# Optimization experiments

Measured on AMD Instinct MI355X. Metric: run time of the kernel, lower is better.

The kernel has to match this reference:

```python
import jax, jax.numpy as jnp
import numpy as np

B, S, H = 2, 1024, 1024        # batch, seq, hidden_size
E, I = 16, 512                 # n_routed_experts, moe_intermediate_size
TOP_K = 2                      # num_experts_per_tok
N_SHARED = 2                   # n_shared_experts -> shared intermediate = I * N_SHARED
SCALE = 1.0                    # routed_scaling_factor
IS = I * N_SHARED


def setup_inputs() -> dict:
    key = jax.random.key(0)
    ks = jax.random.split(key, 8)
    sd = 0.02
    return {
        "hidden_states": jax.random.normal(ks[0], (B, S, H), jnp.float32),
        "gate_w": jax.random.normal(ks[1], (E, H), jnp.float32) * sd,   # router weight [E, H]
        "w_gate": jax.random.normal(ks[2], (E, H, I), jnp.float32) * sd,
        "w_up":   jax.random.normal(ks[3], (E, H, I), jnp.float32) * sd,
        "w_down": jax.random.normal(ks[4], (E, I, H), jnp.float32) * sd,
        "ws_gate": jax.random.normal(ks[5], (H, IS), jnp.float32) * sd,
        "ws_up":   jax.random.normal(ks[6], (H, IS), jnp.float32) * sd,
        "ws_down": jax.random.normal(ks[7], (IS, H), jnp.float32) * sd,
    }


def reference(hidden_states, gate_w, w_gate, w_up, w_down, ws_gate, ws_up, ws_down):
    b, s, h = hidden_states.shape
    x = hidden_states.reshape(-1, h)                      # [T, H]
    T = x.shape[0]

    # ---- gate (greedy top-k over softmax of router logits, fp32) ----
    logits = jnp.einsum('th,eh->te', x.astype(jnp.float32), gate_w.astype(jnp.float32))
    scores = jax.nn.softmax(logits, axis=-1)              # [T, E]
    topk_w, topk_idx = jax.lax.top_k(scores, TOP_K)       # [T, K]
    topk_w = topk_w * SCALE

    # combine weights as dense [T, E] (equivalent to argsort dispatch + scatter combine)
    combine = jnp.zeros((T, E), jnp.float32).at[
        jnp.arange(T)[:, None], topk_idx].add(topk_w)     # [T, E]

    # ---- routed experts: SwiGLU MLP per expert, weighted combine ----
    g = jnp.einsum('th,ehi->tei', x, w_gate)              # [T, E, I]
    u = jnp.einsum('th,ehi->tei', x, w_up)                # [T, E, I]
    act = jax.nn.silu(g) * u                              # [T, E, I]
    # fuse down-proj with combine weights to avoid a [T, E, H] intermediate
    routed = jnp.einsum('tei,eih,te->th', act, w_down, combine)  # [T, H]

    # ---- shared experts on the residual ----
    sg = jax.nn.silu(x @ ws_gate) * (x @ ws_up)           # [T, IS]
    shared = sg @ ws_down                                 # [T, H]

    return (routed + shared).reshape(b, s, h)
```

## Files before the change

### kernel.cpp

```cpp
#include <hip/hip_runtime.h>
#include <hip/hip_bf16.h>

#define T_TOK 2048
#define H_DIM 1024
#define NEXP  16
#define I_DIM 512
#define CAP   384
#define RSCALE 1.0f

typedef unsigned short u16;
typedef unsigned int   u32;
typedef __attribute__((ext_vector_type(4))) float  f32x4;
typedef __attribute__((ext_vector_type(8))) __bf16 bf16x8;
typedef __attribute__((ext_vector_type(8))) u16    u16x8;
typedef __attribute__((ext_vector_type(4))) u16    u16x4;

__device__ __forceinline__ u16 f2bf(float f) {
  u32 u = __builtin_bit_cast(u32, f);
  u32 r = u + 0x7fffu + ((u >> 16) & 1u);
  return (u16)(r >> 16);
}
__device__ __forceinline__ float bf2f(u16 h) {
  return __builtin_bit_cast(float, (u32)h << 16);
}
__device__ __forceinline__ void gload16(const void* g, void* l) {
  __builtin_amdgcn_global_load_lds((const __attribute__((address_space(1))) u32*)g,
                                   (__attribute__((address_space(3))) u32*)l, 16, 0, 0);
}

__device__ __forceinline__ void transpose_tile(const float* __restrict__ src, int srcN,
                                               int k0, int n0,
                                               u16* __restrict__ dst, int dstride, int drow0)
{
  __shared__ float t[64][65];
  int tid = threadIdx.x;
  int kl = tid >> 4, c4 = (tid & 15) * 4;
  #pragma unroll
  for (int p = 0; p < 4; ++p) {
    f32x4 v = *(const f32x4*)(src + (size_t)(k0 + p*16 + kl) * srcN + n0 + c4);
    #pragma unroll
    for (int j = 0; j < 4; ++j) t[p*16 + kl][c4 + j] = v[j];
  }
  __syncthreads();
  int nl = tid >> 3, kc = (tid & 7) * 8;
  #pragma unroll
  for (int p = 0; p < 2; ++p) {
    int n = p*32 + nl;
    u16x8 o;
    #pragma unroll
    for (int j = 0; j < 8; ++j) o[j] = f2bf(t[kc + j][n]);
    *(u16x8*)(dst + (size_t)(drow0 + n) * dstride + k0 + kc) = o;
  }
}

__global__ __launch_bounds__(256) void convert_kernel(
    const float* __restrict__ x,
    const float* __restrict__ w_gate, const float* __restrict__ w_up,
    const float* __restrict__ w_down,
    const float* __restrict__ wsg, const float* __restrict__ wsu,
    const float* __restrict__ wsd,
    u16* __restrict__ xb, u16* __restrict__ wgu_t, u16* __restrict__ wd_t,
    u16* __restrict__ wsgu_t, u16* __restrict__ wsd_t)
{
  int tile = blockIdx.x, tid = threadIdx.x;
  if (tile < 512) {
    #pragma unroll
    for (int p = 0; p < 4; ++p) {
      int fi = tile*1024 + p*256 + tid;
      f32x4 v = ((const f32x4*)x)[fi];
      u16x4 o;
      #pragma unroll
      for (int j = 0; j < 4; ++j) o[j] = f2bf(v[j]);
      ((u16x4*)xb)[fi] = o;
    }
  } else if (tile < 4608) {
    int t2 = tile - 512; int e = t2 >> 8; int r = t2 & 255;
    int mat = r >> 7; int q = r & 127; int kt = q >> 3, nt = q & 7;
    const float* src = (mat ? w_up : w_gate) + (size_t)e * H_DIM * I_DIM;
    transpose_tile(src, I_DIM, kt*64, nt*64,
                   wgu_t + (size_t)e * 1024 * 1024, 1024, mat*512 + nt*64);
  } else if (tile < 6656) {
    int t2 = tile - 4608; int e = t2 >> 7; int q = t2 & 127;
    int kt = q >> 4, nt = q & 15;
    transpose_tile(w_down + (size_t)e * I_DIM * H_DIM, H_DIM, kt*64, nt*64,
                   wd_t + (size_t)e * 1024 * 512, 512, nt*64);
  } else if (tile < 7168) {
    int t2 = tile - 6656; int mat = t2 >> 8; int q = t2 & 255;
    int kt = q >> 4, nt = q & 15;
    transpose_tile(mat ? wsu : wsg, 1024, kt*64, nt*64,
                   wsgu_t, 1024, mat*1024 + nt*64);
  } else {
    int t2 = tile - 7168; int kt = t2 >> 4, nt = t2 & 15;
    transpose_tile(wsd, H_DIM, kt*64, nt*64, wsd_t, 1024, nt*64);
  }
}

__global__ __launch_bounds__(256) void router_kernel(
    const float* __restrict__ x, const float* __restrict__ gw,
    int* __restrict__ perm_tok, int* __restrict__ slot_of,
    float* __restrict__ tok_w, int* __restrict__ counts)
{
  __shared__ f32x4 gws[4096];
  int tid = threadIdx.x;
  const f32x4* gw4 = (const f32x4*)gw;
  #pragma unroll
  for (int i = 0; i < 16; ++i) gws[i*256 + tid] = gw4[i*256 + tid];
  __syncthreads();

  int wv = tid >> 6, l = tid & 63;
  int t0 = blockIdx.x * 16 + wv * 4;

  f32x4 xv[4][4];
  #pragma unroll
  for (int tk = 0; tk < 4; ++tk) {
    const f32x4* xr = (const f32x4*)(x + (size_t)(t0 + tk) * H_DIM);
    #pragma unroll
    for (int j = 0; j < 4; ++j) xv[tk][j] = xr[j*64 + l];
  }

  float p[4][NEXP];
  #pragma unroll
  for (int tk = 0; tk < 4; ++tk)
    #pragma unroll
    for (int e = 0; e < NEXP; ++e) p[tk][e] = 0.f;

  #pragma unroll
  for (int j = 0; j < 4; ++j)
    #pragma unroll
    for (int e = 0; e < NEXP; ++e) {
      f32x4 g = gws[e*256 + j*64 + l];
      #pragma unroll
      for (int tk = 0; tk < 4; ++tk)
        p[tk][e] += xv[tk][j][0]*g[0] + xv[tk][j][1]*g[1]
                  + xv[tk][j][2]*g[2] + xv[tk][j][3]*g[3];
    }

  #pragma unroll
  for (int tk = 0; tk < 4; ++tk)
    #pragma unroll
    for (int e = 0; e < NEXP; ++e)
      #pragma unroll
      for (int off = 32; off; off >>= 1)
        p[tk][e] += __shfl_xor(p[tk][e], off);

  if (l < 4) {
    int tk = l;
    int t = t0 + tk;
    float m = p[tk][0];
    #pragma unroll
    for (int e = 1; e < NEXP; ++e) m = fmaxf(m, p[tk][e]);
    float q[NEXP]; float s = 0.f;
    #pragma unroll
    for (int e = 0; e < NEXP; ++e) { q[e] = expf(p[tk][e] - m); s += q[e]; }
    float inv = 1.f / s;
    int e1 = 0; float b1 = -1.f;
    #pragma unroll
    for (int e = 0; e < NEXP; ++e) if (q[e] > b1) { b1 = q[e]; e1 = e; }
    int e2 = -1; float b2 = -1.f;
    #pragma unroll
    for (int e = 0; e < NEXP; ++e) if (e != e1 && q[e] > b2) { b2 = q[e]; e2 = e; }

    tok_w[2*t]   = b1 * inv * RSCALE;
    tok_w[2*t+1] = b2 * inv * RSCALE;
    int p1 = atomicAdd(&counts[e1], 1);
    if (p1 < CAP) { perm_tok[e1*CAP + p1] = t; slot_of[2*t] = e1*CAP + p1; }
    else slot_of[2*t] = -1;
    int p2 = atomicAdd(&counts[e2], 1);
    if (p2 < CAP) { perm_tok[e2*CAP + p2] = t; slot_of[2*t+1] = e2*CAP + p2; }
    else slot_of[2*t+1] = -1;
  }
}

template<int KDIM, int NMAT, int EPI, bool GATHER, bool EXPERT>
__global__ __launch_bounds__(256, 2) void gemm_kernel(
    const u16* __restrict__ A, const u16* __restrict__ Bt,
    u16* __restrict__ C, float* __restrict__ outF,
    const int* __restrict__ counts, const int* __restrict__ perm_tok, int Mtot)
{
  int e = EXPERT ? blockIdx.z : 0;
  int m_start, m_end;
  if (EXPERT) {
    int cnt = counts[e]; if (cnt > CAP) cnt = CAP;
    m_start = e * CAP; m_end = m_start + cnt;
  } else { m_start = 0; m_end = Mtot; }
  int m0 = m_start + blockIdx.y * 128;
  if (m0 >= m_end) return;
  int n0 = blockIdx.x * 128;
  const u16* Be = Bt + (size_t)e * NMAT * KDIM;

  __shared__ __align__(16) u16 lds[2][2][8192];
  int tid = threadIdx.x;
  int wv = tid >> 6, l = tid & 63;
  int wm = wv >> 1, wn = wv & 1;
  int rl = tid >> 3;
  int c8 = (tid & 7) * 8;

  f32x4 acc[4][4];
  #pragma unroll
  for (int m = 0; m < 4; ++m)
    #pragma unroll
    for (int n = 0; n < 4; ++n) acc[m][n] = f32x4{0.f, 0.f, 0.f, 0.f};

  auto stage = [&](int buf, int kt) {
    int k0 = kt * 64;
    #pragma unroll
    for (int i = 0; i < 4; ++i) {
      int slot = m0 + i*32 + rl;
      int srow = slot < m_end ? slot : m_end - 1;
      int grow = GATHER ? perm_tok[srow] : srow;
      gload16(A + (size_t)grow * KDIM + k0 + c8, &lds[buf][0][i*2048 + wv*512]);
    }
    #pragma unroll
    for (int i = 0; i < 4; ++i) {
      gload16(Be + (size_t)(n0 + i*32 + rl) * KDIM + k0 + c8, &lds[buf][1][i*2048 + wv*512]);
    }
  };

  stage(0, 0);
  __syncthreads();
  const int NK = KDIM / 64;
  for (int kt = 0; kt < NK; ++kt) {
    int buf = kt & 1;
    if (kt + 1 < NK) stage(buf ^ 1, kt + 1);
    const u16* At  = &lds[buf][0][0];
    const u16* Btl = &lds[buf][1][0];
    #pragma unroll
    for (int kk = 0; kk < 2; ++kk) {
      bf16x8 af[4], bv[4];
      int ko = kk*32 + (l >> 4) * 8;
      #pragma unroll
      for (int m = 0; m < 4; ++m)
        af[m] = *(const bf16x8*)(At + (wm*64 + m*16 + (l & 15)) * 64 + ko);
      #pragma unroll
      for (int n = 0; n < 4; ++n)
        bv[n] = *(const bf16x8*)(Btl + (wn*64 + n*16 + (l & 15)) * 64 + ko);
      #pragma unroll
      for (int m = 0; m < 4; ++m)
        #pragma unroll
        for (int n = 0; n < 4; ++n)
          acc[m][n] = __builtin_amdgcn_mfma_f32_16x16x32_bf16(af[m], bv[n], acc[m][n], 0, 0, 0);
    }
    __syncthreads();
  }

  #pragma unroll
  for (int m = 0; m < 4; ++m) {
    #pragma unroll
    for (int n = 0; n < 4; ++n) {
      int col = n0 + wn*64 + n*16 + (l & 15);
      #pragma unroll
      for (int r = 0; r < 4; ++r) {
        int slot = m0 + wm*64 + m*16 + (l >> 4)*4 + r;
        if (slot >= m_end) continue;
        float v = acc[m][n][r];
        if (EPI == 0) C[(size_t)slot * NMAT + col] = f2bf(v);
        else          outF[(size_t)slot * H_DIM + col] = v;
      }
    }
  }
}

__global__ __launch_bounds__(256) void silumul_s_kernel(
    const u16* __restrict__ gu_s, u16* __restrict__ act_s)
{
  int idx = blockIdx.x * 256 + threadIdx.x;
  int s = idx >> 7;
  int i8 = (idx & 127) * 8;
  u16x8 g = *(const u16x8*)(gu_s + (size_t)s*2048 + i8);
  u16x8 u = *(const u16x8*)(gu_s + (size_t)s*2048 + 1024 + i8);
  u16x8 o;
  #pragma unroll
  for (int j = 0; j < 8; ++j) {
    float gf = bf2f(g[j]), uf = bf2f(u[j]);
    o[j] = f2bf(gf / (1.f + expf(-gf)) * uf);
  }
  *(u16x8*)(act_s + (size_t)s*1024 + i8) = o;
}

__global__ __launch_bounds__(256) void silumul_r_kernel(
    const u16* __restrict__ gu_r, u16* __restrict__ act_r,
    const int* __restrict__ counts)
{
  int idx = blockIdx.x * 256 + threadIdx.x;
  int s = idx >> 6;
  int i8 = (idx & 63) * 8;
  int e = s / CAP, pos = s - e * CAP;
  if (pos >= counts[e]) return;
  u16x8 g = *(const u16x8*)(gu_r + (size_t)s*1024 + i8);
  u16x8 u = *(const u16x8*)(gu_r + (size_t)s*1024 + 512 + i8);
  u16x8 o;
  #pragma unroll
  for (int j = 0; j < 8; ++j) {
    float gf = bf2f(g[j]), uf = bf2f(u[j]);
    o[j] = f2bf(gf / (1.f + expf(-gf)) * uf);
  }
  *(u16x8*)(act_r + (size_t)s*I_DIM + i8) = o;
}

__global__ __launch_bounds__(256) void combine_kernel(
    float* __restrict__ out, const float* __restrict__ down_r,
    const int* __restrict__ slot_of, const float* __restrict__ tok_w)
{
  int t = blockIdx.x, c = threadIdx.x;
  f32x4* orow = (f32x4*)(out + (size_t)t * H_DIM);
  f32x4 o = orow[c];
  int s0 = slot_of[2*t], s1 = slot_of[2*t+1];
  float w0 = tok_w[2*t], w1 = tok_w[2*t+1];
  if (s0 >= 0) {
    f32x4 v = ((const f32x4*)(down_r + (size_t)s0 * H_DIM))[c];
    o += v * w0;
  }
  if (s1 >= 0) {
    f32x4 v = ((const f32x4*)(down_r + (size_t)s1 * H_DIM))[c];
    o += v * w1;
  }
  orow[c] = o;
}

extern "C" void kernel_launch(void* const* d_in, const int* in_sizes, int n_in,
                              void* d_out, int out_size, void* d_ws, size_t ws_size,
                              hipStream_t stream)
{
  (void)in_sizes; (void)n_in; (void)out_size;
  const float* x       = (const float*)d_in[0];
  const float* gate_w  = (const float*)d_in[1];
  const float* w_gate  = (const float*)d_in[2];
  const float* w_up    = (const float*)d_in[3];
  const float* w_down  = (const float*)d_in[4];
  const float* wsg     = (const float*)d_in[5];
  const float* wsu     = (const float*)d_in[6];
  const float* wsd     = (const float*)d_in[7];
  float* out = (float*)d_out;

  char* base = (char*)d_ws;
  size_t off = 0;
  auto alloc = [&](size_t n) -> void* {
    void* r = base + off;
    off += (n + 255) & ~(size_t)255;
    return r;
  };
  u16* xb       = (u16*)alloc((size_t)T_TOK * H_DIM * 2);
  u16* wgu_t    = (u16*)alloc((size_t)NEXP * 1024 * 1024 * 2);
  u16* wd_t     = (u16*)alloc((size_t)NEXP * 1024 * 512 * 2);
  u16* wsgu_t   = (u16*)alloc((size_t)2048 * 1024 * 2);
  u16* wsd_t    = (u16*)alloc((size_t)1024 * 1024 * 2);
  u16* gu_r     = (u16*)alloc((size_t)NEXP * CAP * 1024 * 2);
  u16* gu_s     = (u16*)alloc((size_t)2048 * 2048 * 2);
  int*   counts   = (int*)alloc(64);
  int*   tok_w_i  = (int*)alloc((size_t)2 * T_TOK * 4);
  int*   slot_of  = (int*)alloc((size_t)2 * T_TOK * 4);
  int*   perm_tok = (int*)alloc((size_t)NEXP * CAP * 4);
  float* tok_w = (float*)tok_w_i;
  u16*   act_s  = xb;
  u16*   act_r  = gu_s;
  float* down_r = (float*)wgu_t;
  if (off > ws_size) return;

  hipMemsetAsync(counts, 0, 64, stream);
  convert_kernel<<<7424, 256, 0, stream>>>(x, w_gate, w_up, w_down, wsg, wsu, wsd,
                                           xb, wgu_t, wd_t, wsgu_t, wsd_t);
  router_kernel<<<128, 256, 0, stream>>>(x, gate_w, perm_tok, slot_of, tok_w, counts);
  gemm_kernel<1024, 1024, 0, true,  true ><<<dim3(8, CAP/128, NEXP), 256, 0, stream>>>(
      xb, wgu_t, gu_r, nullptr, counts, perm_tok, 0);
  gemm_kernel<1024, 2048, 0, false, false><<<dim3(16, 16, 1), 256, 0, stream>>>(
      xb, wsgu_t, gu_s, nullptr, counts, perm_tok, T_TOK);
  silumul_s_kernel<<<1024, 256, 0, stream>>>(gu_s, act_s);
  silumul_r_kernel<<<NEXP*CAP*64/256, 256, 0, stream>>>(gu_r, act_r, counts);
  gemm_kernel<1024, 1024, 2, false, false><<<dim3(8, 16, 1), 256, 0, stream>>>(
      act_s, wsd_t, nullptr, out, counts, perm_tok, T_TOK);
  gemm_kernel< 512, 1024, 2, false, true ><<<dim3(8, CAP/128, NEXP), 256, 0, stream>>>(
      act_r, wd_t, nullptr, down_r, counts, perm_tok, 0);
  combine_kernel<<<T_TOK, 256, 0, stream>>>(out, down_r, slot_of, tok_w);
}
```

Before: 281.1 us.

## Merge routed and shared expert GEMMs into single grouped launches

Combines the routed-expert and shared-expert gate/up GEMMs into one launch with a flat block index dispatching to either problem, and does the same for the two down-projection GEMMs and the two SiLU-mul kernels. This removes several kernel launches and lets the partially empty routed tiles overlap with shared-expert tiles instead of leaving the GPU underfilled between launches. The routed activation buffer moves into the freed converted-weight region. Kernel dimensions become runtime values, which may cost some compile-time specialization in the inner loop.

```diff
diff --git a/kernel.cpp b/kernel.cpp
--- a/kernel.cpp
+++ b/kernel.cpp
@@ -171,22 +171,54 @@
   }
 }
 
-template<int KDIM, int NMAT, int EPI, bool GATHER, bool EXPERT>
-__global__ __launch_bounds__(256, 2) void gemm_kernel(
-    const u16* __restrict__ A, const u16* __restrict__ Bt,
-    u16* __restrict__ C, float* __restrict__ outF,
-    const int* __restrict__ counts, const int* __restrict__ perm_tok, int Mtot)
-{
-  int e = EXPERT ? blockIdx.z : 0;
-  int m_start, m_end;
-  if (EXPERT) {
+template<bool GU>
+__global__ __launch_bounds__(256, 2) void gemm_fused_kernel(
+    const u16* __restrict__ A_sh, const u16* __restrict__ A_rt,
+    const u16* __restrict__ B_sh, const u16* __restrict__ B_rt,
+    u16* __restrict__ C_sh, u16* __restrict__ C_rt,
+    float* __restrict__ O_sh, float* __restrict__ O_rt,
+    const int* __restrict__ counts, const int* __restrict__ perm_tok)
+{
+  int b = blockIdx.x;
+  bool routed = b < 384;
+
+  int kdim, m0, m_end, n0, cstr;
+  const u16 *A, *B;
+  u16* C; float* O;
+  bool gather = false;
+
+  if (routed) {
+    int e  = b / 24;
+    int r  = b % 24;
+    int my = r >> 3, nx = r & 7;
     int cnt = counts[e]; if (cnt > CAP) cnt = CAP;
-    m_start = e * CAP; m_end = m_start + cnt;
-  } else { m_start = 0; m_end = Mtot; }
-  int m0 = m_start + blockIdx.y * 128;
-  if (m0 >= m_end) return;
-  int n0 = blockIdx.x * 128;
-  const u16* Be = Bt + (size_t)e * NMAT * KDIM;
+    int m_start = e * CAP;
+    m_end = m_start + cnt;
+    m0 = m_start + my * 128;
+    if (m0 >= m_end) return;
+    n0 = nx * 128;
+    if (GU) {
+      kdim = 1024; A = A_rt; gather = true;
+      B = B_rt + ((size_t)e << 20);
+      C = C_rt; cstr = 1024; O = nullptr;
+    } else {
+      kdim = 512;  A = A_rt;
+      B = B_rt + ((size_t)e << 19);
+      C = nullptr; cstr = 0; O = O_rt;
+    }
+  } else {
+    int s = b - 384;
+    kdim = 1024;
+    if (GU) {
+      int my = s >> 4, nx = s & 15;
+      m0 = my * 128; n0 = nx * 128; m_end = T_TOK;
+      A = A_sh; B = B_sh; C = C_sh; cstr = 2048; O = nullptr;
+    } else {
+      int my = s >> 3, nx = s & 7;
+      m0 = my * 128; n0 = nx * 128; m_end = T_TOK;
+      A = A_sh; B = B_sh; C = nullptr; cstr = 0; O = O_sh;
+    }
+  }
 
   __shared__ __align__(16) u16 lds[2][2][8192];
   int tid = threadIdx.x;
@@ -207,18 +239,18 @@
     for (int i = 0; i < 4; ++i) {
       int slot = m0 + i*32 + rl;
       int srow = slot < m_end ? slot : m_end - 1;
-      int grow = GATHER ? perm_tok[srow] : srow;
-      gload16(A + (size_t)grow * KDIM + k0 + c8, &lds[buf][0][i*2048 + wv*512]);
+      int grow = gather ? perm_tok[srow] : srow;
+      gload16(A + (size_t)grow * kdim + k0 + c8, &lds[buf][0][i*2048 + wv*512]);
     }
     #pragma unroll
     for (int i = 0; i < 4; ++i) {
-      gload16(Be + (size_t)(n0 + i*32 + rl) * KDIM + k0 + c8, &lds[buf][1][i*2048 + wv*512]);
+      gload16(B + (size_t)(n0 + i*32 + rl) * kdim + k0 + c8, &lds[buf][1][i*2048 + wv*512]);
     }
   };
 
   stage(0, 0);
   __syncthreads();
-  const int NK = KDIM / 64;
+  const int NK = kdim >> 6;
   for (int kt = 0; kt < NK; ++kt) {
     int buf = kt & 1;
     if (kt + 1 < NK) stage(buf ^ 1, kt + 1);
@@ -253,48 +285,48 @@
         int slot = m0 + wm*64 + m*16 + (l >> 4)*4 + r;
         if (slot >= m_end) continue;
         float v = acc[m][n][r];
-        if (EPI == 0) C[(size_t)slot * NMAT + col] = f2bf(v);
-        else          outF[(size_t)slot * H_DIM + col] = v;
+        if (GU) C[(size_t)slot * cstr + col] = f2bf(v);
+        else    O[(size_t)slot * H_DIM + col] = v;
       }
     }
   }
 }
 
-__global__ __launch_bounds__(256) void silumul_s_kernel(
-    const u16* __restrict__ gu_s, u16* __restrict__ act_s)
-{
-  int idx = blockIdx.x * 256 + threadIdx.x;
-  int s = idx >> 7;
-  int i8 = (idx & 127) * 8;
-  u16x8 g = *(const u16x8*)(gu_s + (size_t)s*2048 + i8);
-  u16x8 u = *(const u16x8*)(gu_s + (size_t)s*2048 + 1024 + i8);
-  u16x8 o;
-  #pragma unroll
-  for (int j = 0; j < 8; ++j) {
-    float gf = bf2f(g[j]), uf = bf2f(u[j]);
-    o[j] = f2bf(gf / (1.f + expf(-gf)) * uf);
-  }
-  *(u16x8*)(act_s + (size_t)s*1024 + i8) = o;
-}
-
-__global__ __launch_bounds__(256) void silumul_r_kernel(
-    const u16* __restrict__ gu_r, u16* __restrict__ act_r,
+__global__ __launch_bounds__(256) void silumul_kernel(
+    const u16* __restrict__ gu_r, const u16* __restrict__ gu_s,
+    u16* __restrict__ act_r, u16* __restrict__ act_s,
     const int* __restrict__ counts)
 {
-  int idx = blockIdx.x * 256 + threadIdx.x;
-  int s = idx >> 6;
-  int i8 = (idx & 63) * 8;
-  int e = s / CAP, pos = s - e * CAP;
-  if (pos >= counts[e]) return;
-  u16x8 g = *(const u16x8*)(gu_r + (size_t)s*1024 + i8);
-  u16x8 u = *(const u16x8*)(gu_r + (size_t)s*1024 + 512 + i8);
-  u16x8 o;
-  #pragma unroll
-  for (int j = 0; j < 8; ++j) {
-    float gf = bf2f(g[j]), uf = bf2f(u[j]);
-    o[j] = f2bf(gf / (1.f + expf(-gf)) * uf);
-  }
-  *(u16x8*)(act_r + (size_t)s*I_DIM + i8) = o;
+  int b = blockIdx.x;
+  if (b < 1536) {
+    int idx = b * 256 + threadIdx.x;
+    int s = idx >> 6;
+    int i8 = (idx & 63) * 8;
+    int e = s / CAP, pos = s - e * CAP;
+    if (pos >= counts[e]) return;
+    u16x8 g = *(const u16x8*)(gu_r + (size_t)s*1024 + i8);
+    u16x8 u = *(const u16x8*)(gu_r + (size_t)s*1024 + 512 + i8);
+    u16x8 o;
+    #pragma unroll
+    for (int j = 0; j < 8; ++j) {
+      float gf = bf2f(g[j]), uf = bf2f(u[j]);
+      o[j] = f2bf(gf / (1.f + expf(-gf)) * uf);
+    }
+    *(u16x8*)(act_r + (size_t)s*I_DIM + i8) = o;
+  } else {
+    int idx = (b - 1536) * 256 + threadIdx.x;
+    int s = idx >> 7;
+    int i8 = (idx & 127) * 8;
+    u16x8 g = *(const u16x8*)(gu_s + (size_t)s*2048 + i8);
+    u16x8 u = *(const u16x8*)(gu_s + (size_t)s*2048 + 1024 + i8);
+    u16x8 o;
+    #pragma unroll
+    for (int j = 0; j < 8; ++j) {
+      float gf = bf2f(g[j]), uf = bf2f(u[j]);
+      o[j] = f2bf(gf / (1.f + expf(-gf)) * uf);
+    }
+    *(u16x8*)(act_s + (size_t)s*1024 + i8) = o;
+  }
 }
 
 __global__ __launch_bounds__(256) void combine_kernel(
@@ -352,23 +384,18 @@
   int*   perm_tok = (int*)alloc((size_t)NEXP * CAP * 4);
   float* tok_w = (float*)tok_w_i;
   u16*   act_s  = xb;
-  u16*   act_r  = gu_s;
   float* down_r = (float*)wgu_t;
+  u16*   act_r  = (u16*)((char*)wgu_t + (24u<<20));
   if (off > ws_size) return;
 
   hipMemsetAsync(counts, 0, 64, stream);
   convert_kernel<<<7424, 256, 0, stream>>>(x, w_gate, w_up, w_down, wsg, wsu, wsd,
                                            xb, wgu_t, wd_t, wsgu_t, wsd_t);
   router_kernel<<<128, 256, 0, stream>>>(x, gate_w, perm_tok, slot_of, tok_w, counts);
-  gemm_kernel<1024, 1024, 0, true,  true ><<<dim3(8, CAP/128, NEXP), 256, 0, stream>>>(
-      xb, wgu_t, gu_r, nullptr, counts, perm_tok, 0);
-  gemm_kernel<1024, 2048, 0, false, false><<<dim3(16, 16, 1), 256, 0, stream>>>(
-      xb, wsgu_t, gu_s, nullptr, counts, perm_tok, T_TOK);
-  silumul_s_kernel<<<1024, 256, 0, stream>>>(gu_s, act_s);
-  silumul_r_kernel<<<NEXP*CAP*64/256, 256, 0, stream>>>(gu_r, act_r, counts);
-  gemm_kernel<1024, 1024, 2, false, false><<<dim3(8, 16, 1), 256, 0, stream>>>(
-      act_s, wsd_t, nullptr, out, counts, perm_tok, T_TOK);
-  gemm_kernel< 512, 1024, 2, false, true ><<<dim3(8, CAP/128, NEXP), 256, 0, stream>>>(
-      act_r, wd_t, nullptr, down_r, counts, perm_tok, 0);
+  gemm_fused_kernel<true><<<640, 256, 0, stream>>>(
+      xb, xb, wsgu_t, wgu_t, gu_s, gu_r, nullptr, nullptr, counts, perm_tok);
+  silumul_kernel<<<2560, 256, 0, stream>>>(gu_r, gu_s, act_r, act_s, counts);
+  gemm_fused_kernel<false><<<512, 256, 0, stream>>>(
+      act_s, act_r, wsd_t, wd_t, nullptr, nullptr, out, down_r, counts, perm_tok);
   combine_kernel<<<T_TOK, 256, 0, stream>>>(out, down_r, slot_of, tok_w);
 }
```

Result: faster. 268.8 us (-4.4%).
